# Kernel tuning notes

Hardware: AMD Instinct MI355X
Metric: run time of the kernel (lower is better)

Reference implementation:

```python
import jax, jax.numpy as jnp
import numpy as np
from jax import lax

D_MODEL = 512
CLASS_NUM = 8000
MAX_LEN = 80
VOCAB = 8002  # len(char2idx): chars + sos/eos
SOS_IDX = 0


def setup_inputs() -> dict:
    key = jax.random.key(0)
    ks = jax.random.split(key, 16)
    T, B, D, V, C = 128, 128, D_MODEL, VOCAB, CLASS_NUM
    s = 1.0 / np.sqrt(D)
    inp = {
        "inputs": jax.random.normal(ks[0], (T, B, D), jnp.float32),
        # additive attention params (query_size=key_size=hidden_size=D)
        "Wq": jax.random.normal(ks[1], (D, D), jnp.float32) * s,
        "bq": jnp.zeros((D,), jnp.float32),
        "Wk": jax.random.normal(ks[2], (D, D), jnp.float32) * s,
        "bk": jnp.zeros((D,), jnp.float32),
        "v": jax.random.normal(ks[3], (D,), jnp.float32) * s,
        # GRUCell: input_size = 2*D, hidden_size = D (PyTorch layout)
        "W_ih": jax.random.normal(ks[4], (3 * D, 2 * D), jnp.float32) * s,
        "b_ih": jnp.zeros((3 * D,), jnp.float32),
        "W_hh": jax.random.normal(ks[5], (3 * D, D), jnp.float32) * s,
        "b_hh": jnp.zeros((3 * D,), jnp.float32),
        # embedding table and classifier
        "emb": jax.random.normal(ks[6], (V, D), jnp.float32),
        "Wc": jax.random.normal(ks[7], (C, D), jnp.float32) * s,
        "bc": jnp.zeros((C,), jnp.float32),
    }
    return inp


def _gru_cell(x, h, W_ih, b_ih, W_hh, b_hh):
    # PyTorch GRUCell math
    gi = x @ W_ih.T + b_ih  # [B, 3D]
    gh = h @ W_hh.T + b_hh  # [B, 3D]
    i_r, i_z, i_n = jnp.split(gi, 3, axis=1)
    h_r, h_z, h_n = jnp.split(gh, 3, axis=1)
    r = jax.nn.sigmoid(i_r + h_r)
    z = jax.nn.sigmoid(i_z + h_z)
    n = jnp.tanh(i_n + r * h_n)
    return (1.0 - z) * n + z * h


def reference(inputs, Wq, bq, Wk, bk, v, W_ih, b_ih, W_hh, b_hh, emb, Wc, bc):
    T, B, D = inputs.shape
    # Attention is called as attention(inputs, keys) with keys = inputs each
    # step -> weights are loop-invariant; compute the context once.
    e = jnp.tanh(inputs @ Wq.T + bq + inputs @ Wk.T + bk) @ v  # [T, B]
    att = jax.nn.softmax(e, axis=0)[..., None]  # [T, B, 1]
    c = jnp.sum(att * inputs, axis=0)  # [B, D]

    h0 = inputs[0]  # initial GRU hidden = first encoder frame
    out0 = emb[jnp.full((B,), SOS_IDX, dtype=jnp.int32)]  # sos embedding

    def step(carry, _):
        h, out = carry
        x = jnp.concatenate([out, c], axis=1)  # [B, 2D]
        h = _gru_cell(x, h, W_ih, b_ih, W_hh, b_hh)
        pred = h @ Wc.T + bc  # [B, class_num]
        top1 = jnp.argmax(pred, axis=1)  # greedy decode (eval mode)
        return (h, emb[top1]), pred

    _, preds = lax.scan(step, (h0, out0), None, length=MAX_LEN)
    return preds  # [max_len, B, class_num]
```

## Files before the change

kernel.cpp:

```cpp
#include <hip/hip_runtime.h>
#include <cstdint>
#include <cstddef>

#define D_MOD 512
#define TH3   1536
#define CLS   8000
#define MAXLEN 80
#define B_SZ  128
#define T_LEN 128
#define NK0   16
#define EGI_ROWS 8000

typedef __attribute__((ext_vector_type(8))) __bf16 bf16x8;
typedef __attribute__((ext_vector_type(8))) unsigned short u16x8;
typedef __attribute__((ext_vector_type(4))) float f32x4;

__device__ __forceinline__ unsigned short f2bf(float x) {
    unsigned u = __float_as_uint(x);
    unsigned r = ((u >> 16) & 1u) + 0x7fffu;
    return (unsigned short)((u + r) >> 16);
}
__device__ __forceinline__ float bf2f(unsigned short h) {
    return __uint_as_float(((unsigned)h) << 16);
}
__device__ __forceinline__ f32x4 mfma16(u16x8 a, u16x8 b, f32x4 c) {
    return __builtin_amdgcn_mfma_f32_16x16x32_bf16(
        __builtin_bit_cast(bf16x8, a), __builtin_bit_cast(bf16x8, b), c, 0, 0, 0);
}
__device__ __forceinline__ void conv8(const float* __restrict__ p, u16x8& hi, u16x8& lo) {
    float4 f0 = *(const float4*)p;
    float4 f1 = *(const float4*)(p + 4);
    float fs[8] = {f0.x, f0.y, f0.z, f0.w, f1.x, f1.y, f1.z, f1.w};
    #pragma unroll
    for (int j = 0; j < 8; ++j) {
        unsigned short h = f2bf(fs[j]);
        hi[j] = h;
        lo[j] = f2bf(fs[j] - bf2f(h));
    }
}
__device__ __forceinline__ unsigned long long packkey(float v, int n) {
    unsigned u = __float_as_uint(v);
    u = (u & 0x80000000u) ? ~u : (u | 0x80000000u);
    return ((unsigned long long)u << 32) | (unsigned)(~(unsigned)n);
}
__device__ __forceinline__ unsigned long long shfl_xor_u64(unsigned long long x, int mask) {
    unsigned lo = (unsigned)x, hi = (unsigned)(x >> 32);
    lo = __shfl_xor(lo, mask, 16);
    hi = __shfl_xor(hi, mask, 16);
    return ((unsigned long long)hi << 32) | lo;
}
__device__ __forceinline__ size_t pk_off(int n, int k) {
    int tile = n >> 4, lr = n & 15, k0i = k >> 5, lk = (k >> 3) & 3, e = k & 7;
    return ((size_t)(tile * NK0 + k0i) * 64 + (lk * 16 + lr)) * 8 + e;
}

__global__ __launch_bounds__(256) void cvt2p_kernel(
    const float* __restrict__ s1, const float* __restrict__ s2, int ld,
    long total4, unsigned short* __restrict__ hi, unsigned short* __restrict__ lo)
{
    long i4 = (long)blockIdx.x * 256 + threadIdx.x;
    if (i4 >= total4) return;
    long r = i4 >> 7;
    int c = (int)(i4 & 127) * 4;
    float4 a = *(const float4*)(s1 + r * (long)ld + c);
    if (s2) {
        float4 b = *(const float4*)(s2 + r * (long)ld + c);
        a.x += b.x; a.y += b.y; a.z += b.z; a.w += b.w;
    }
    float xs[4] = {a.x, a.y, a.z, a.w};
    unsigned short hs[4], ls[4];
    #pragma unroll
    for (int j = 0; j < 4; ++j) {
        hs[j] = f2bf(xs[j]);
        ls[j] = f2bf(xs[j] - bf2f(hs[j]));
    }
    size_t o = pk_off((int)r, c);
    *(ushort4*)(hi + o) = make_ushort4(hs[0], hs[1], hs[2], hs[3]);
    *(ushort4*)(lo + o) = make_ushort4(ls[0], ls[1], ls[2], ls[3]);
}

template<bool GATHER_CONV, bool CONVB, bool ADD2D, bool ARGMAX, int NS, int KS>
__device__ __forceinline__ void gemm_ks2(
    float* __restrict__ red,
    const unsigned short* __restrict__ Ahi, const unsigned short* __restrict__ Alo,
    const float* __restrict__ Afp, const unsigned long long* __restrict__ gslot,
    const unsigned short* __restrict__ Bhi, const unsigned short* __restrict__ Blo,
    const float* __restrict__ Bfp,
    const float* __restrict__ bias, const float* __restrict__ D2,
    float* __restrict__ C, int ldc,
    unsigned long long* __restrict__ aslot, int bx, int by)
{
    static_assert(NS * KS == 8, "8 waves per block");
    const int tid = threadIdx.x;
    const int w = tid >> 6, lane = tid & 63;
    const int lr = lane & 15, lk = lane >> 4;
    const int ns = w % NS, ks = w / NS;
    const int m0 = by * 16;
    const int n0 = (bx * NS + ns) * 32;
    const int tA = by;
    const int tB0 = n0 >> 4, tB1 = tB0 + 1;

    const float* paf = nullptr;
    if constexpr (GATHER_CONV) {
        int g = gslot ? (int)(~(unsigned)gslot[m0 + lr]) : (m0 + lr);
        paf = Afp + (size_t)g * D_MOD + lk * 8;
    }
    const float *pb0f = nullptr, *pb1f = nullptr;
    if constexpr (CONVB) {
        pb0f = Bfp + (size_t)(n0 + lr) * D_MOD + lk * 8;
        pb1f = Bfp + (size_t)(n0 + 16 + lr) * D_MOD + lk * 8;
    }

    f32x4 acc0 = (f32x4){0.f, 0.f, 0.f, 0.f};
    f32x4 acc1 = (f32x4){0.f, 0.f, 0.f, 0.f};

    const int kBeg = ks * (NK0 / KS), kEnd = kBeg + (NK0 / KS);
    for (int k0i = kBeg; k0i < kEnd; ++k0i) {
        u16x8 ah, al, b0h, b0l, b1h, b1l;
        if constexpr (GATHER_CONV) {
            conv8(paf + k0i * 32, ah, al);
        } else {
            size_t oA = ((size_t)(tA * NK0 + k0i) * 64 + lane) * 8;
            ah = *(const u16x8*)(Ahi + oA); al = *(const u16x8*)(Alo + oA);
        }
        if constexpr (CONVB) {
            conv8(pb0f + k0i * 32, b0h, b0l);
            conv8(pb1f + k0i * 32, b1h, b1l);
        } else {
            size_t oB0 = ((size_t)(tB0 * NK0 + k0i) * 64 + lane) * 8;
            size_t oB1 = ((size_t)(tB1 * NK0 + k0i) * 64 + lane) * 8;
            b0h = *(const u16x8*)(Bhi + oB0); b0l = *(const u16x8*)(Blo + oB0);
            b1h = *(const u16x8*)(Bhi + oB1); b1l = *(const u16x8*)(Blo + oB1);
        }
        acc0 = mfma16(ah, b0h, acc0);
        acc0 = mfma16(ah, b0l, acc0);
        acc0 = mfma16(al, b0h, acc0);
        acc1 = mfma16(ah, b1h, acc1);
        acc1 = mfma16(ah, b1l, acc1);
        acc1 = mfma16(al, b1h, acc1);
    }

    float af[8];
    #pragma unroll
    for (int i = 0; i < 4; ++i) { af[i] = acc0[i]; af[4 + i] = acc1[i]; }

    if (ks > 0) {
        const int slot = (ks - 1) * NS + ns;
        #pragma unroll
        for (int i = 0; i < 8; ++i) red[slot * 576 + lane * 9 + i] = af[i];
    }
    __syncthreads();
    if (ks == 0) {
        #pragma unroll
        for (int j = 1; j < KS; ++j) {
            const int slot = (j - 1) * NS + ns;
            #pragma unroll
            for (int i = 0; i < 8; ++i) af[i] += red[slot * 576 + lane * 9 + i];
        }
        #pragma unroll
        for (int r = 0; r < 4; ++r) {
            const int row = m0 + lk * 4 + r;
            unsigned long long kmax = 0ull;
            #pragma unroll
            for (int ni = 0; ni < 2; ++ni) {
                const int col = n0 + ni * 16 + lr;
                float val = af[ni * 4 + r];
                if (bias) val += bias[col];
                if constexpr (ADD2D) val += D2[(size_t)row * ldc + col];
                C[(size_t)row * ldc + col] = val;
                if constexpr (ARGMAX) {
                    unsigned long long k = packkey(val, col);
                    if (k > kmax) kmax = k;
                }
            }
            if constexpr (ARGMAX) {
                #pragma unroll
                for (int off = 1; off < 16; off <<= 1) {
                    unsigned long long o = shfl_xor_u64(kmax, off);
                    if (o > kmax) kmax = o;
                }
                if (lr == 0) atomicMax(&aslot[row], kmax);
            }
        }
    }
}

template<int G>
__device__ __forceinline__ bool xcd_map(int p, int& bx, int& by) {
    int x = p & 7, s = p >> 3;
    by = s & 7;
    bx = x * G + (s >> 3);
    return true;
}

__global__ __launch_bounds__(512) void egi_kernel(
    const float* __restrict__ emb,
    const unsigned short* __restrict__ WihaHi, const unsigned short* __restrict__ WihaLo,
    float* __restrict__ Egi)
{
    __shared__ float red[7 * 576];
    int p = blockIdx.x;
    int x = p & 7, s = p >> 3;
    int by = s % 500, bx = x * 6 + s / 500;
    gemm_ks2<true, false, false, false, 1, 8>(red, nullptr, nullptr, emb, nullptr,
        WihaHi, WihaLo, nullptr, nullptr, nullptr, Egi, TH3, nullptr, bx, by);
}

__global__ __launch_bounds__(512) void gh_kernel(
    const unsigned short* __restrict__ hHi, const unsigned short* __restrict__ hLo,
    const unsigned short* __restrict__ WhhHi, const unsigned short* __restrict__ WhhLo,
    const float* __restrict__ b_hh, float* __restrict__ gh)
{
    __shared__ float red[7 * 576];
    int bx, by;
    xcd_map<6>(blockIdx.x, bx, by);
    gemm_ks2<false, false, false, false, 1, 8>(red, hHi, hLo, nullptr, nullptr,
        WhhHi, WhhLo, nullptr, b_hh, nullptr, gh, TH3, nullptr, bx, by);
}

template<bool CONVB>
__global__ __launch_bounds__(512) void cls_gh_kernel(
    const unsigned short* __restrict__ hHi, const unsigned short* __restrict__ hLo,
    const unsigned short* __restrict__ WcHi, const unsigned short* __restrict__ WcLo,
    const float* __restrict__ Wc, const float* __restrict__ bc,
    float* __restrict__ C, unsigned long long* __restrict__ aslot,
    const unsigned short* __restrict__ WhhHi, const unsigned short* __restrict__ WhhLo,
    const float* __restrict__ b_hh, float* __restrict__ gh)
{
    __shared__ float red[7 * 576];
    const int p = blockIdx.x;
    if (p < 1024) {
        int bx, by;
        xcd_map<16>(p, bx, by);
        if (bx >= 125) return;
        gemm_ks2<false, CONVB, false, true, 2, 4>(red, hHi, hLo, nullptr, nullptr,
            WcHi, WcLo, Wc, bc, nullptr, C, CLS, aslot, bx, by);
    } else {
        int bx, by;
        xcd_map<6>(p - 1024, bx, by);
        gemm_ks2<false, false, false, false, 1, 8>(red, hHi, hLo, nullptr, nullptr,
            WhhHi, WhhLo, nullptr, b_hh, nullptr, gh, TH3, nullptr, bx, by);
    }
}

__global__ __launch_bounds__(512) void step_dual_kernel(
    const unsigned short* __restrict__ hHi, const unsigned short* __restrict__ hLo,
    const unsigned short* __restrict__ WhhHi, const unsigned short* __restrict__ WhhLo,
    const float* __restrict__ b_hh,
    const float* __restrict__ emb, const unsigned long long* __restrict__ sPrev,
    const unsigned short* __restrict__ WihaHi, const unsigned short* __restrict__ WihaLo,
    const float* __restrict__ gc,
    float* __restrict__ gh, float* __restrict__ gi)
{
    __shared__ float red[7 * 576];
    int p = blockIdx.x;
    const int z = (p >= 384);
    p -= z * 384;
    int bx, by;
    xcd_map<6>(p, bx, by);
    if (z == 0)
        gemm_ks2<false, false, false, false, 1, 8>(red, hHi, hLo, nullptr, nullptr,
            WhhHi, WhhLo, nullptr, b_hh, nullptr, gh, TH3, nullptr, bx, by);
    else
        gemm_ks2<true, false, true, false, 1, 8>(red, nullptr, nullptr, emb, sPrev,
            WihaHi, WihaLo, nullptr, nullptr, gc, gi, TH3, nullptr, bx, by);
}

__global__ __launch_bounds__(512) void gemm128_kernel(
    const unsigned short* __restrict__ Ahi, const unsigned short* __restrict__ Alo,
    const unsigned short* __restrict__ Bhi, const unsigned short* __restrict__ Blo,
    const float* __restrict__ bias, float* __restrict__ C)
{
    __shared__ float red[7 * 576];
    int bx, by;
    xcd_map<6>(blockIdx.x, bx, by);
    gemm_ks2<false, false, false, false, 1, 8>(red, Ahi, Alo, nullptr, nullptr,
        Bhi, Blo, nullptr, bias, nullptr, C, TH3, nullptr, bx, by);
}

template<bool CONVB>
__global__ __launch_bounds__(512) void cls_kernel(
    const unsigned short* __restrict__ hHi, const unsigned short* __restrict__ hLo,
    const unsigned short* __restrict__ WcHi, const unsigned short* __restrict__ WcLo,
    const float* __restrict__ Wc, const float* __restrict__ bc,
    float* __restrict__ C, unsigned long long* __restrict__ aslot)
{
    __shared__ float red[3 * 2 * 576];
    int bx, by;
    xcd_map<16>(blockIdx.x, bx, by);
    if (bx >= 125) return;
    gemm_ks2<false, CONVB, false, true, 2, 4>(red, hHi, hLo, nullptr, nullptr,
        WcHi, WcLo, Wc, bc, nullptr, C, CLS, aslot, bx, by);
}

__global__ __launch_bounds__(256) void attn_e_mfma(
    const float* __restrict__ inp,
    const unsigned short* __restrict__ WqkHi, const unsigned short* __restrict__ WqkLo,
    const float* __restrict__ bq, const float* __restrict__ bk,
    const float* __restrict__ v, float* __restrict__ e)
{
    __shared__ __align__(16) unsigned short Ah[32][40];
    __shared__ __align__(16) unsigned short Al[32][40];
    __shared__ float red[4][32];
    const int tid = threadIdx.x, w = tid >> 6, lane = tid & 63;
    const int lr = lane & 15, lk = lane >> 4;
    const int m0 = blockIdx.x * 32;
    const int srow = tid >> 3, scol = (tid & 7) * 4;

    f32x4 acc[2][8];
    #pragma unroll
    for (int i = 0; i < 2; ++i)
        #pragma unroll
        for (int j = 0; j < 8; ++j) acc[i][j] = (f32x4){0.f, 0.f, 0.f, 0.f};

    for (int k0i = 0; k0i < NK0; ++k0i) {
        float4 x = *(const float4*)(inp + (size_t)(m0 + srow) * D_MOD + k0i * 32 + scol);
        float xs[4] = {x.x, x.y, x.z, x.w};
        #pragma unroll
        for (int j = 0; j < 4; ++j) {
            unsigned short h = f2bf(xs[j]);
            Ah[srow][scol + j] = h;
            Al[srow][scol + j] = f2bf(xs[j] - bf2f(h));
        }
        __syncthreads();
        u16x8 a[2][2];
        #pragma unroll
        for (int mi = 0; mi < 2; ++mi) {
            a[mi][0] = *(const u16x8*)&Ah[mi * 16 + lr][lk * 8];
            a[mi][1] = *(const u16x8*)&Al[mi * 16 + lr][lk * 8];
        }
        #pragma unroll
        for (int nf = 0; nf < 8; ++nf) {
            const int tile = w * 8 + nf;
            size_t ob = ((size_t)(tile * NK0 + k0i) * 64 + lane) * 8;
            u16x8 bh = *(const u16x8*)(WqkHi + ob);
            u16x8 bl = *(const u16x8*)(WqkLo + ob);
            #pragma unroll
            for (int mi = 0; mi < 2; ++mi) {
                acc[mi][nf] = mfma16(a[mi][0], bh, acc[mi][nf]);
                acc[mi][nf] = mfma16(a[mi][0], bl, acc[mi][nf]);
                acc[mi][nf] = mfma16(a[mi][1], bh, acc[mi][nf]);
            }
        }
        __syncthreads();
    }

    float ep[2][4];
    #pragma unroll
    for (int mi = 0; mi < 2; ++mi)
        #pragma unroll
        for (int r = 0; r < 4; ++r) ep[mi][r] = 0.f;
    #pragma unroll
    for (int nf = 0; nf < 8; ++nf) {
        const int col = w * 128 + nf * 16 + lr;
        const float bb = bq[col] + bk[col];
        const float vv = v[col];
        #pragma unroll
        for (int mi = 0; mi < 2; ++mi)
            #pragma unroll
            for (int r = 0; r < 4; ++r)
                ep[mi][r] += vv * tanhf(acc[mi][nf][r] + bb);
    }
    #pragma unroll
    for (int mi = 0; mi < 2; ++mi)
        #pragma unroll
        for (int r = 0; r < 4; ++r) {
            float s = ep[mi][r];
            #pragma unroll
            for (int off = 1; off < 16; off <<= 1) s += __shfl_xor(s, off, 16);
            if (lr == 0) red[w][mi * 16 + lk * 4 + r] = s;
        }
    __syncthreads();
    if (tid < 32) e[m0 + tid] = red[0][tid] + red[1][tid] + red[2][tid] + red[3][tid];
}

__global__ __launch_bounds__(256) void softmax_ctx_kernel(
    const float* __restrict__ inp, const float* __restrict__ e,
    unsigned short* __restrict__ cHi, unsigned short* __restrict__ cLo,
    float* __restrict__ h1, unsigned short* __restrict__ h1Hi, unsigned short* __restrict__ h1Lo,
    unsigned long long* __restrict__ slots)
{
    __shared__ float att[T_LEN];
    __shared__ float red;
    const int b = blockIdx.x, tid = threadIdx.x;
    float val = -1e30f;
    if (tid < T_LEN) { val = e[(size_t)tid * B_SZ + b]; att[tid] = val; }
    __syncthreads();
    if (tid < 64) {
        float m = fmaxf(att[tid], att[tid + 64]);
        #pragma unroll
        for (int off = 32; off; off >>= 1) m = fmaxf(m, __shfl_xor(m, off));
        if (tid == 0) red = m;
    }
    __syncthreads();
    const float mx = red;
    __syncthreads();
    if (tid < T_LEN) att[tid] = expf(val - mx);
    __syncthreads();
    if (tid < 64) {
        float s = att[tid] + att[tid + 64];
        #pragma unroll
        for (int off = 32; off; off >>= 1) s += __shfl_xor(s, off);
        if (tid == 0) red = s;
    }
    __syncthreads();
    const float inv = 1.f / red;

    const int d0 = tid * 2;
    float ax = 0.f, ay = 0.f;
    for (int t = 0; t < T_LEN; ++t) {
        float a = att[t];
        float2 x = *(const float2*)(inp + ((size_t)t * B_SZ + b) * D_MOD + d0);
        ax += a * x.x; ay += a * x.y;
        if (t == 0) {
            *(float2*)(h1 + (size_t)b * D_MOD + d0) = x;
            unsigned short hx = f2bf(x.x), hy = f2bf(x.y);
            h1Hi[pk_off(b, d0)]     = hx;
            h1Hi[pk_off(b, d0 + 1)] = hy;
            h1Lo[pk_off(b, d0)]     = f2bf(x.x - bf2f(hx));
            h1Lo[pk_off(b, d0 + 1)] = f2bf(x.y - bf2f(hy));
        }
    }
    ax *= inv; ay *= inv;
    unsigned short cx = f2bf(ax), cy = f2bf(ay);
    cHi[pk_off(b, d0)]     = cx;
    cHi[pk_off(b, d0 + 1)] = cy;
    cLo[pk_off(b, d0)]     = f2bf(ax - bf2f(cx));
    cLo[pk_off(b, d0 + 1)] = f2bf(ay - bf2f(cy));
    if (tid == 0) {
        slots[b] = 0ull;
        slots[B_SZ + b] = 0x00000000FFFFFFFFull;
    }
}

__global__ __launch_bounds__(512) void gru_combine(
    const float* __restrict__ gh, const float* __restrict__ gi,
    const float* __restrict__ hPrev, float* __restrict__ hCur,
    unsigned short* __restrict__ hHiC, unsigned short* __restrict__ hLoC,
    unsigned long long* __restrict__ slotCur)
{
    const int b = blockIdx.x, k = threadIdx.x;
    const float* gib = gi + (size_t)b * TH3;
    const float* ghb = gh + (size_t)b * TH3;
    float r = 1.f / (1.f + expf(-(gib[k] + ghb[k])));
    float z = 1.f / (1.f + expf(-(gib[k + 512] + ghb[k + 512])));
    float n = tanhf(gib[k + 1024] + r * ghb[k + 1024]);
    float h = hPrev[(size_t)b * D_MOD + k];
    float hv = (1.f - z) * n + z * h;
    hCur[(size_t)b * D_MOD + k] = hv;
    unsigned short hh = f2bf(hv);
    size_t o = pk_off(b, k);
    hHiC[o] = hh;
    hLoC[o] = f2bf(hv - bf2f(hh));
    if (k == 0) slotCur[b] = 0ull;
}

__global__ __launch_bounds__(512) void gru_combine_egi(
    const float* __restrict__ gh, const float* __restrict__ Egi,
    const float* __restrict__ gc, const unsigned long long* __restrict__ sPrev,
    const float* __restrict__ hPrev, float* __restrict__ hCur,
    unsigned short* __restrict__ hHiC, unsigned short* __restrict__ hLoC,
    unsigned long long* __restrict__ slotCur)
{
    const int b = blockIdx.x, k = threadIdx.x;
    const int sel = (int)(~(unsigned)sPrev[b]);
    const float* gib = Egi + (size_t)sel * TH3;
    const float* gcb = gc + (size_t)b * TH3;
    const float* ghb = gh + (size_t)b * TH3;
    float gi0 = gib[k] + gcb[k];
    float gi1 = gib[k + 512] + gcb[k + 512];
    float gi2 = gib[k + 1024] + gcb[k + 1024];
    float r = 1.f / (1.f + expf(-(gi0 + ghb[k])));
    float z = 1.f / (1.f + expf(-(gi1 + ghb[k + 512])));
    float n = tanhf(gi2 + r * ghb[k + 1024]);
    float h = hPrev[(size_t)b * D_MOD + k];
    float hv = (1.f - z) * n + z * h;
    hCur[(size_t)b * D_MOD + k] = hv;
    unsigned short hh = f2bf(hv);
    size_t o = pk_off(b, k);
    hHiC[o] = hh;
    hLoC[o] = f2bf(hv - bf2f(hh));
    if (k == 0) slotCur[b] = 0ull;
}

extern "C" void kernel_launch(void* const* d_in, const int* in_sizes, int n_in,
                              void* d_out, int out_size, void* d_ws, size_t ws_size,
                              hipStream_t stream)
{
    const float* inp  = (const float*)d_in[0];
    const float* Wq   = (const float*)d_in[1];
    const float* bq   = (const float*)d_in[2];
    const float* Wk   = (const float*)d_in[3];
    const float* bk   = (const float*)d_in[4];
    const float* v    = (const float*)d_in[5];
    const float* W_ih = (const float*)d_in[6];
    const float* b_ih = (const float*)d_in[7];
    const float* W_hh = (const float*)d_in[8];
    const float* b_hh = (const float*)d_in[9];
    const float* emb  = (const float*)d_in[10];
    const float* Wc   = (const float*)d_in[11];
    const float* bc   = (const float*)d_in[12];
    float* out = (float*)d_out;

    char* base = (char*)d_ws;
    size_t off = 0;
    auto alloc = [&](size_t bytes) -> char* {
        char* q = base + off;
        off += (bytes + 255) & ~(size_t)255;
        return q;
    };
    typedef unsigned short us;
    us* WqkHi  = (us*)alloc(512 * 512 * 2);
    us* WqkLo  = (us*)alloc(512 * 512 * 2);
    us* WhhHi  = (us*)alloc((size_t)TH3 * 512 * 2);
    us* WhhLo  = (us*)alloc((size_t)TH3 * 512 * 2);
    us* WihaHi = (us*)alloc((size_t)TH3 * 512 * 2);
    us* WihaLo = (us*)alloc((size_t)TH3 * 512 * 2);
    us* WihbHi = (us*)alloc((size_t)TH3 * 512 * 2);
    us* WihbLo = (us*)alloc((size_t)TH3 * 512 * 2);
    float* e   = (float*)alloc(T_LEN * B_SZ * 4);
    us* cHi    = (us*)alloc(B_SZ * 512 * 2);
    us* cLo    = (us*)alloc(B_SZ * 512 * 2);
    float* gc  = (float*)alloc((size_t)B_SZ * TH3 * 4);
    float* gh  = (float*)alloc((size_t)B_SZ * TH3 * 4);
    float* gi  = (float*)alloc((size_t)B_SZ * TH3 * 4);
    float* hF[2]; us* hHi[2]; us* hLo[2];
    hF[0] = (float*)alloc(B_SZ * 512 * 4);
    hF[1] = (float*)alloc(B_SZ * 512 * 4);
    hHi[0] = (us*)alloc(B_SZ * 512 * 2);
    hHi[1] = (us*)alloc(B_SZ * 512 * 2);
    hLo[0] = (us*)alloc(B_SZ * 512 * 2);
    hLo[1] = (us*)alloc(B_SZ * 512 * 2);
    unsigned long long* slots = (unsigned long long*)alloc(2 * B_SZ * 8);
    us* WcHi = (us*)alloc((size_t)CLS * 512 * 2);
    us* WcLo = (us*)alloc((size_t)CLS * 512 * 2);
    const bool PREB = (off <= ws_size);
    float* Egi = (float*)alloc((size_t)EGI_ROWS * TH3 * 4);
    const bool EGIB = (off <= ws_size);

    cvt2p_kernel<<<(512 * 128) / 256, 256, 0, stream>>>(Wq, Wk, 512, 512L * 128, WqkHi, WqkLo);
    cvt2p_kernel<<<(TH3 * 128) / 256, 256, 0, stream>>>(W_hh, nullptr, 512, (long)TH3 * 128, WhhHi, WhhLo);
    cvt2p_kernel<<<(TH3 * 128) / 256, 256, 0, stream>>>(W_ih, nullptr, 1024, (long)TH3 * 128, WihaHi, WihaLo);
    cvt2p_kernel<<<(TH3 * 128) / 256, 256, 0, stream>>>(W_ih + 512, nullptr, 1024, (long)TH3 * 128, WihbHi, WihbLo);
    if (PREB)
        cvt2p_kernel<<<(CLS * 128) / 256, 256, 0, stream>>>(Wc, nullptr, 512, (long)CLS * 128, WcHi, WcLo);
    if (EGIB)
        egi_kernel<<<8 * 6 * 500, 512, 0, stream>>>(emb, WihaHi, WihaLo, Egi);

    attn_e_mfma<<<(T_LEN * B_SZ) / 32, 256, 0, stream>>>(inp, WqkHi, WqkLo, bq, bk, v, e);
    softmax_ctx_kernel<<<B_SZ, 256, 0, stream>>>(inp, e, cHi, cLo, hF[1], hHi[1], hLo[1], slots);
    gemm128_kernel<<<384, 512, 0, stream>>>(cHi, cLo, WihbHi, WihbLo, b_ih, gc);

    if (EGIB) {
        gh_kernel<<<384, 512, 0, stream>>>(hHi[1], hLo[1], WhhHi, WhhLo, b_hh, gh);
        for (int t = 0; t < MAXLEN; ++t) {
            const int pi = (t + 1) & 1, ci = t & 1;
            unsigned long long* sPrev = slots + pi * B_SZ;
            unsigned long long* sCur  = slots + ci * B_SZ;

            gru_combine_egi<<<B_SZ, 512, 0, stream>>>(
                gh, Egi, gc, sPrev, hF[pi], hF[ci], hHi[ci], hLo[ci], sCur);
            if (PREB)
                cls_gh_kernel<false><<<1408, 512, 0, stream>>>(
                    hHi[ci], hLo[ci], WcHi, WcLo, nullptr, bc,
                    out + (size_t)t * B_SZ * CLS, sCur,
                    WhhHi, WhhLo, b_hh, gh);
            else
                cls_gh_kernel<true><<<1408, 512, 0, stream>>>(
                    hHi[ci], hLo[ci], nullptr, nullptr, Wc, bc,
                    out + (size_t)t * B_SZ * CLS, sCur,
                    WhhHi, WhhLo, b_hh, gh);
        }
    } else {
        for (int t = 0; t < MAXLEN; ++t) {
            const int pi = (t + 1) & 1, ci = t & 1;
            unsigned long long* sPrev = slots + pi * B_SZ;
            unsigned long long* sCur  = slots + ci * B_SZ;

            step_dual_kernel<<<768, 512, 0, stream>>>(
                hHi[pi], hLo[pi], WhhHi, WhhLo, b_hh,
                emb, sPrev, WihaHi, WihaLo, gc, gh, gi);
            gru_combine<<<B_SZ, 512, 0, stream>>>(
                gh, gi, hF[pi], hF[ci], hHi[ci], hLo[ci], sCur);
            if (PREB)
                cls_kernel<false><<<1024, 512, 0, stream>>>(
                    hHi[ci], hLo[ci], WcHi, WcLo, nullptr, bc,
                    out + (size_t)t * B_SZ * CLS, sCur);
            else
                cls_kernel<true><<<1024, 512, 0, stream>>>(
                    hHi[ci], hLo[ci], nullptr, nullptr, Wc, bc,
                    out + (size_t)t * B_SZ * CLS, sCur);
        }
    }
}
```

Baseline: 2.615 ms.

## Tile multiple M sub-tiles per wave in classifier GEMM and use nontemporal stores

Templates the shared split-K MFMA GEMM on an M-tile count so each wave computes several 16-row tiles and reuses each loaded B fragment across them. A new fused classifier plus hidden-projection kernel with 608 blocks replaces the 1408-block launch when both precomputed buffers fit, which cuts repeated reads of the large Wc weights. Output logits can be written with nontemporal stores so they do not evict weights from cache. In exchange each wave holds more accumulators and uses more reduction shared memory, which can lower occupancy.

```diff
diff --git a/kernel.cpp b/kernel.cpp
--- a/kernel.cpp
+++ b/kernel.cpp
@@ -79,7 +79,8 @@
     *(ushort4*)(lo + o) = make_ushort4(ls[0], ls[1], ls[2], ls[3]);
 }
 
-template<bool GATHER_CONV, bool CONVB, bool ADD2D, bool ARGMAX, int NS, int KS>
+template<bool GATHER_CONV, bool CONVB, bool ADD2D, bool ARGMAX, bool NT,
+         int NS, int KS, int MT>
 __device__ __forceinline__ void gemm_ks2(
     float* __restrict__ red,
     const unsigned short* __restrict__ Ahi, const unsigned short* __restrict__ Alo,
@@ -91,13 +92,14 @@
     unsigned long long* __restrict__ aslot, int bx, int by)
 {
     static_assert(NS * KS == 8, "8 waves per block");
+    static_assert(!GATHER_CONV || MT == 1, "gather path is MT=1 only");
     const int tid = threadIdx.x;
     const int w = tid >> 6, lane = tid & 63;
     const int lr = lane & 15, lk = lane >> 4;
     const int ns = w % NS, ks = w / NS;
-    const int m0 = by * 16;
+    const int m0 = by * (16 * MT);
     const int n0 = (bx * NS + ns) * 32;
-    const int tA = by;
+    const int tA0 = by * MT;
     const int tB0 = n0 >> 4, tB1 = tB0 + 1;
 
     const float* paf = nullptr;
@@ -111,17 +113,25 @@
         pb1f = Bfp + (size_t)(n0 + 16 + lr) * D_MOD + lk * 8;
     }
 
-    f32x4 acc0 = (f32x4){0.f, 0.f, 0.f, 0.f};
-    f32x4 acc1 = (f32x4){0.f, 0.f, 0.f, 0.f};
+    f32x4 acc[MT][2];
+    #pragma unroll
+    for (int mi = 0; mi < MT; ++mi) {
+        acc[mi][0] = (f32x4){0.f, 0.f, 0.f, 0.f};
+        acc[mi][1] = (f32x4){0.f, 0.f, 0.f, 0.f};
+    }
 
     const int kBeg = ks * (NK0 / KS), kEnd = kBeg + (NK0 / KS);
     for (int k0i = kBeg; k0i < kEnd; ++k0i) {
-        u16x8 ah, al, b0h, b0l, b1h, b1l;
+        u16x8 ah[MT], al[MT], b0h, b0l, b1h, b1l;
         if constexpr (GATHER_CONV) {
-            conv8(paf + k0i * 32, ah, al);
+            conv8(paf + k0i * 32, ah[0], al[0]);
         } else {
-            size_t oA = ((size_t)(tA * NK0 + k0i) * 64 + lane) * 8;
-            ah = *(const u16x8*)(Ahi + oA); al = *(const u16x8*)(Alo + oA);
+            #pragma unroll
+            for (int mi = 0; mi < MT; ++mi) {
+                size_t oA = ((size_t)((tA0 + mi) * NK0 + k0i) * 64 + lane) * 8;
+                ah[mi] = *(const u16x8*)(Ahi + oA);
+                al[mi] = *(const u16x8*)(Alo + oA);
+            }
         }
         if constexpr (CONVB) {
             conv8(pb0f + k0i * 32, b0h, b0l);
@@ -132,22 +142,30 @@
             b0h = *(const u16x8*)(Bhi + oB0); b0l = *(const u16x8*)(Blo + oB0);
             b1h = *(const u16x8*)(Bhi + oB1); b1l = *(const u16x8*)(Blo + oB1);
         }
-        acc0 = mfma16(ah, b0h, acc0);
-        acc0 = mfma16(ah, b0l, acc0);
-        acc0 = mfma16(al, b0h, acc0);
-        acc1 = mfma16(ah, b1h, acc1);
-        acc1 = mfma16(ah, b1l, acc1);
-        acc1 = mfma16(al, b1h, acc1);
-    }
-
-    float af[8];
-    #pragma unroll
-    for (int i = 0; i < 4; ++i) { af[i] = acc0[i]; af[4 + i] = acc1[i]; }
+        #pragma unroll
+        for (int mi = 0; mi < MT; ++mi) {
+            acc[mi][0] = mfma16(ah[mi], b0h, acc[mi][0]);
+            acc[mi][0] = mfma16(ah[mi], b0l, acc[mi][0]);
+            acc[mi][0] = mfma16(al[mi], b0h, acc[mi][0]);
+            acc[mi][1] = mfma16(ah[mi], b1h, acc[mi][1]);
+            acc[mi][1] = mfma16(ah[mi], b1l, acc[mi][1]);
+            acc[mi][1] = mfma16(al[mi], b1h, acc[mi][1]);
+        }
+    }
+
+    float af[MT][8];
+    #pragma unroll
+    for (int mi = 0; mi < MT; ++mi)
+        #pragma unroll
+        for (int i = 0; i < 4; ++i) { af[mi][i] = acc[mi][0][i]; af[mi][4 + i] = acc[mi][1][i]; }
 
     if (ks > 0) {
         const int slot = (ks - 1) * NS + ns;
         #pragma unroll
-        for (int i = 0; i < 8; ++i) red[slot * 576 + lane * 9 + i] = af[i];
+        for (int mi = 0; mi < MT; ++mi)
+            #pragma unroll
+            for (int i = 0; i < 8; ++i)
+                red[(slot * MT + mi) * 576 + lane * 9 + i] = af[mi][i];
     }
     __syncthreads();
     if (ks == 0) {
@@ -155,31 +173,38 @@
         for (int j = 1; j < KS; ++j) {
             const int slot = (j - 1) * NS + ns;
             #pragma unroll
-            for (int i = 0; i < 8; ++i) af[i] += red[slot * 576 + lane * 9 + i];
-        }
-        #pragma unroll
-        for (int r = 0; r < 4; ++r) {
-            const int row = m0 + lk * 4 + r;
-            unsigned long long kmax = 0ull;
+            for (int mi = 0; mi < MT; ++mi)
+                #pragma unroll
+                for (int i = 0; i < 8; ++i)
+                    af[mi][i] += red[(slot * MT + mi) * 576 + lane * 9 + i];
+        }
+        #pragma unroll
+        for (int mi = 0; mi < MT; ++mi) {
             #pragma unroll
-            for (int ni = 0; ni < 2; ++ni) {
-                const int col = n0 + ni * 16 + lr;
-                float val = af[ni * 4 + r];
-                if (bias) val += bias[col];
-                if constexpr (ADD2D) val += D2[(size_t)row * ldc + col];
-                C[(size_t)row * ldc + col] = val;
+            for (int r = 0; r < 4; ++r) {
+                const int row = m0 + mi * 16 + lk * 4 + r;
+                unsigned long long kmax = 0ull;
+                #pragma unroll
+                for (int ni = 0; ni < 2; ++ni) {
+                    const int col = n0 + ni * 16 + lr;
+                    float val = af[mi][ni * 4 + r];
+                    if (bias) val += bias[col];
+                    if constexpr (ADD2D) val += D2[(size_t)row * ldc + col];
+                    if constexpr (NT) __builtin_nontemporal_store(val, &C[(size_t)row * ldc + col]);
+                    else C[(size_t)row * ldc + col] = val;
+                    if constexpr (ARGMAX) {
+                        unsigned long long k = packkey(val, col);
+                        if (k > kmax) kmax = k;
+                    }
+                }
                 if constexpr (ARGMAX) {
-                    unsigned long long k = packkey(val, col);
-                    if (k > kmax) kmax = k;
+                    #pragma unroll
+                    for (int off = 1; off < 16; off <<= 1) {
+                        unsigned long long o = shfl_xor_u64(kmax, off);
+                        if (o > kmax) kmax = o;
+                    }
+                    if (lr == 0) atomicMax(&aslot[row], kmax);
                 }
-            }
-            if constexpr (ARGMAX) {
-                #pragma unroll
-                for (int off = 1; off < 16; off <<= 1) {
-                    unsigned long long o = shfl_xor_u64(kmax, off);
-                    if (o > kmax) kmax = o;
-                }
-                if (lr == 0) atomicMax(&aslot[row], kmax);
             }
         }
     }
@@ -193,276 +218,14 @@
     return true;
 }
 
-__global__ __launch_bounds__(512) void egi_kernel(
-    const float* __restrict__ emb,
-    const unsigned short* __restrict__ WihaHi, const unsigned short* __restrict__ WihaLo,
-    float* __restrict__ Egi)
-{
-    __shared__ float red[7 * 576];
-    int p = blockIdx.x;
-    int x = p & 7, s = p >> 3;
-    int by = s % 500, bx = x * 6 + s / 500;
-    gemm_ks2<true, false, false, false, 1, 8>(red, nullptr, nullptr, emb, nullptr,
-        WihaHi, WihaLo, nullptr, nullptr, nullptr, Egi, TH3, nullptr, bx, by);
-}
-
-__global__ __launch_bounds__(512) void gh_kernel(
-    const unsigned short* __restrict__ hHi, const unsigned short* __restrict__ hLo,
-    const unsigned short* __restrict__ WhhHi, const unsigned short* __restrict__ WhhLo,
-    const float* __restrict__ b_hh, float* __restrict__ gh)
-{
-    __shared__ float red[7 * 576];
-    int bx, by;
-    xcd_map<6>(blockIdx.x, bx, by);
-    gemm_ks2<false, false, false, false, 1, 8>(red, hHi, hLo, nullptr, nullptr,
-        WhhHi, WhhLo, nullptr, b_hh, nullptr, gh, TH3, nullptr, bx, by);
-}
-
-template<bool CONVB>
-__global__ __launch_bounds__(512) void cls_gh_kernel(
-    const unsigned short* __restrict__ hHi, const unsigned short* __restrict__ hLo,
-    const unsigned short* __restrict__ WcHi, const unsigned short* __restrict__ WcLo,
-    const float* __restrict__ Wc, const float* __restrict__ bc,
-    float* __restrict__ C, unsigned long long* __restrict__ aslot,
-    const unsigned short* __restrict__ WhhHi, const unsigned short* __restrict__ WhhLo,
-    const float* __restrict__ b_hh, float* __restrict__ gh)
-{
-    __shared__ float red[7 * 576];
-    const int p = blockIdx.x;
-    if (p < 1024) {
-        int bx, by;
-        xcd_map<16>(p, bx, by);
-        if (bx >= 125) return;
-        gemm_ks2<false, CONVB, false, true, 2, 4>(red, hHi, hLo, nullptr, nullptr,
-            WcHi, WcLo, Wc, bc, nullptr, C, CLS, aslot, bx, by);
-    } else {
-        int bx, by;
-        xcd_map<6>(p - 1024, bx, by);
-        gemm_ks2<false, false, false, false, 1, 8>(red, hHi, hLo, nullptr, nullptr,
-            WhhHi, WhhLo, nullptr, b_hh, nullptr, gh, TH3, nullptr, bx, by);
-    }
-}
-
-__global__ __launch_bounds__(512) void step_dual_kernel(
-    const unsigned short* __restrict__ hHi, const unsigned short* __restrict__ hLo,
-    const unsigned short* __restrict__ WhhHi, const unsigned short* __restrict__ WhhLo,
-    const float* __restrict__ b_hh,
-    const float* __restrict__ emb, const unsigned long long* __restrict__ sPrev,
-    const unsigned short* __restrict__ WihaHi, const unsigned short* __restrict__ WihaLo,
-    const float* __restrict__ gc,
-    float* __restrict__ gh, float* __restrict__ gi)
-{
-    __shared__ float red[7 * 576];
-    int p = blockIdx.x;
-    const int z = (p >= 384);
-    p -= z * 384;
-    int bx, by;
-    xcd_map<6>(p, bx, by);
-    if (z == 0)
-        gemm_ks2<false, false, false, false, 1, 8>(red, hHi, hLo, nullptr, nullptr,
-            WhhHi, WhhLo, nullptr, b_hh, nullptr, gh, TH3, nullptr, bx, by);
-    else
-        gemm_ks2<true, false, true, false, 1, 8>(red, nullptr, nullptr, emb, sPrev,
-            WihaHi, WihaLo, nullptr, nullptr, gc, gi, TH3, nullptr, bx, by);
-}
-
-__global__ __launch_bounds__(512) void gemm128_kernel(
-    const unsigned short* __restrict__ Ahi, const unsigned short* __restrict__ Alo,
-    const unsigned short* __restrict__ Bhi, const unsigned short* __restrict__ Blo,
-    const float* __restrict__ bias, float* __restrict__ C)
-{
-    __shared__ float red[7 * 576];
-    int bx, by;
-    xcd_map<6>(blockIdx.x, bx, by);
-    gemm_ks2<false, false, false, false, 1, 8>(red, Ahi, Alo, nullptr, nullptr,
-        Bhi, Blo, nullptr, bias, nullptr, C, TH3, nullptr, bx, by);
-}
-
-template<bool CONVB>
-__global__ __launch_bounds__(512) void cls_kernel(
-    const unsigned short* __restrict__ hHi, const unsigned short* __restrict__ hLo,
-    const unsigned short* __restrict__ WcHi, const unsigned short* __restrict__ WcLo,
-    const float* __restrict__ Wc, const float* __restrict__ bc,
-    float* __restrict__ C, unsigned long long* __restrict__ aslot)
-{
-    __shared__ float red[3 * 2 * 576];
-    int bx, by;
-    xcd_map<16>(blockIdx.x, bx, by);
-    if (bx >= 125) return;
-    gemm_ks2<false, CONVB, false, true, 2, 4>(red, hHi, hLo, nullptr, nullptr,
-        WcHi, WcLo, Wc, bc, nullptr, C, CLS, aslot, bx, by);
-}
-
-__global__ __launch_bounds__(256) void attn_e_mfma(
-    const float* __restrict__ inp,
-    const unsigned short* __restrict__ WqkHi, const unsigned short* __restrict__ WqkLo,
-    const float* __restrict__ bq, const float* __restrict__ bk,
-    const float* __restrict__ v, float* __restrict__ e)
-{
-    __shared__ __align__(16) unsigned short Ah[32][40];
-    __shared__ __align__(16) unsigned short Al[32][40];
-    __shared__ float red[4][32];
-    const int tid = threadIdx.x, w = tid >> 6, lane = tid & 63;
-    const int lr = lane & 15, lk = lane >> 4;
-    const int m0 = blockIdx.x * 32;
-    const int srow = tid >> 3, scol = (tid & 7) * 4;
-
-    f32x4 acc[2][8];
-    #pragma unroll
-    for (int i = 0; i < 2; ++i)
-        #pragma unroll
-        for (int j = 0; j < 8; ++j) acc[i][j] = (f32x4){0.f, 0.f, 0.f, 0.f};
-
-    for (int k0i = 0; k0i < NK0; ++k0i) {
-        float4 x = *(const float4*)(inp + (size_t)(m0 + srow) * D_MOD + k0i * 32 + scol);
-        float xs[4] = {x.x, x.y, x.z, x.w};
-        #pragma unroll
-        for (int j = 0; j < 4; ++j) {
-            unsigned short h = f2bf(xs[j]);
-            Ah[srow][scol + j] = h;
-            Al[srow][scol + j] = f2bf(xs[j] - bf2f(h));
-        }
-        __syncthreads();
-        u16x8 a[2][2];
-        #pragma unroll
-        for (int mi = 0; mi < 2; ++mi) {
-            a[mi][0] = *(const u16x8*)&Ah[mi * 16 + lr][lk * 8];
-            a[mi][1] = *(const u16x8*)&Al[mi * 16 + lr][lk * 8];
-        }
-        #pragma unroll
-        for (int nf = 0; nf < 8; ++nf) {
-            const int tile = w * 8 + nf;
-            size_t ob = ((size_t)(tile * NK0 + k0i) * 64 + lane) * 8;
-            u16x8 bh = *(const u16x8*)(WqkHi + ob);
-            u16x8 bl = *(const u16x8*)(WqkLo + ob);
-            #pragma unroll
-            for (int mi = 0; mi < 2; ++mi) {
-                acc[mi][nf] = mfma16(a[mi][0], bh, acc[mi][nf]);
-                acc[mi][nf] = mfma16(a[mi][0], bl, acc[mi][nf]);
-                acc[mi][nf] = mfma16(a[mi][1], bh, acc[mi][nf]);
-            }
-        }
-        __syncthreads();
-    }
-
-    float ep[2][4];
-    #pragma unroll
-    for (int mi = 0; mi < 2; ++mi)
-        #pragma unroll
-        for (int r = 0; r < 4; ++r) ep[mi][r] = 0.f;
-    #pragma unroll
-    for (int nf = 0; nf < 8; ++nf) {
-        const int col = w * 128 + nf * 16 + lr;
-        const float bb = bq[col] + bk[col];
-        const float vv = v[col];
-        #pragma unroll
-        for (int mi = 0; mi < 2; ++mi)
-            #pragma unroll
-            for (int r = 0; r < 4; ++r)
-                ep[mi][r] += vv * tanhf(acc[mi][nf][r] + bb);
-    }
-    #pragma unroll
-    for (int mi = 0; mi < 2; ++mi)
-        #pragma unroll
-        for (int r = 0; r < 4; ++r) {
-            float s = ep[mi][r];
-            #pragma unroll
-            for (int off = 1; off < 16; off <<= 1) s += __shfl_xor(s, off, 16);
-            if (lr == 0) red[w][mi * 16 + lk * 4 + r] = s;
-        }
-    __syncthreads();
-    if (tid < 32) e[m0 + tid] = red[0][tid] + red[1][tid] + red[2][tid] + red[3][tid];
-}
-
-__global__ __launch_bounds__(256) void softmax_ctx_kernel(
-    const float* __restrict__ inp, const float* __restrict__ e,
-    unsigned short* __restrict__ cHi, unsigned short* __restrict__ cLo,
-    float* __restrict__ h1, unsigned short* __restrict__ h1Hi, unsigned short* __restrict__ h1Lo,
-    unsigned long long* __restrict__ slots)
-{
-    __shared__ float att[T_LEN];
-    __shared__ float red;
-    const int b = blockIdx.x, tid = threadIdx.x;
-    float val = -1e30f;
-    if (tid < T_LEN) { val = e[(size_t)tid * B_SZ + b]; att[tid] = val; }
-    __syncthreads();
-    if (tid < 64) {
-        float m = fmaxf(att[tid], att[tid + 64]);
-        #pragma unroll
-        for (int off = 32; off; off >>= 1) m = fmaxf(m, __shfl_xor(m, off));
-        if (tid == 0) red = m;
-    }
-    __syncthreads();
-    const float mx = red;
-    __syncthreads();
-    if (tid < T_LEN) att[tid] = expf(val - mx);
-    __syncthreads();
-    if (tid < 64) {
-        float s = att[tid] + att[tid + 64];
-        #pragma unroll
-        for (int off = 32; off; off >>= 1) s += __shfl_xor(s, off);
-        if (tid == 0) red = s;
-    }
-    __syncthreads();
-    const float inv = 1.f / red;
-
-    const int d0 = tid * 2;
-    float ax = 0.f, ay = 0.f;
-    for (int t = 0; t < T_LEN; ++t) {
-        float a = att[t];
-        float2 x = *(const float2*)(inp + ((size_t)t * B_SZ + b) * D_MOD + d0);
-        ax += a * x.x; ay += a * x.y;
-        if (t == 0) {
-            *(float2*)(h1 + (size_t)b * D_MOD + d0) = x;
-            unsigned short hx = f2bf(x.x), hy = f2bf(x.y);
-            h1Hi[pk_off(b, d0)]     = hx;
-            h1Hi[pk_off(b, d0 + 1)] = hy;
-            h1Lo[pk_off(b, d0)]     = f2bf(x.x - bf2f(hx));
-            h1Lo[pk_off(b, d0 + 1)] = f2bf(x.y - bf2f(hy));
-        }
-    }
-    ax *= inv; ay *= inv;
-    unsigned short cx = f2bf(ax), cy = f2bf(ay);
-    cHi[pk_off(b, d0)]     = cx;
-    cHi[pk_off(b, d0 + 1)] = cy;
-    cLo[pk_off(b, d0)]     = f2bf(ax - bf2f(cx));
-    cLo[pk_off(b, d0 + 1)] = f2bf(ay - bf2f(cy));
-    if (tid == 0) {
-        slots[b] = 0ull;
-        slots[B_SZ + b] = 0x00000000FFFFFFFFull;
-    }
-}
-
-__global__ __launch_bounds__(512) void gru_combine(
-    const float* __restrict__ gh, const float* __restrict__ gi,
-    const float* __restrict__ hPrev, float* __restrict__ hCur,
-    unsigned short* __restrict__ hHiC, unsigned short* __restrict__ hLoC,
-    unsigned long long* __restrict__ slotCur)
-{
-    const int b = blockIdx.x, k = threadIdx.x;
-    const float* gib = gi + (size_t)b * TH3;
-    const float* ghb = gh + (size_t)b * TH3;
-    float r = 1.f / (1.f + expf(-(gib[k] + ghb[k])));
-    float z = 1.f / (1.f + expf(-(gib[k + 512] + ghb[k + 512])));
-    float n = tanhf(gib[k + 1024] + r * ghb[k + 1024]);
-    float h = hPrev[(size_t)b * D_MOD + k];
-    float hv = (1.f - z) * n + z * h;
-    hCur[(size_t)b * D_MOD + k] = hv;
-    unsigned short hh = f2bf(hv);
-    size_t o = pk_off(b, k);
-    hHiC[o] = hh;
-    hLoC[o] = f2bf(hv - bf2f(hh));
-    if (k == 0) slotCur[b] = 0ull;
-}
-
-__global__ __launch_bounds__(512) void gru_combine_egi(
-    const float* __restrict__ gh, const float* __restrict__ Egi,
+__device__ __forceinline__ void gru_job_egi(
+    int b, const float* __restrict__ gh, const float* __restrict__ Egi,
     const float* __restrict__ gc, const unsigned long long* __restrict__ sPrev,
     const float* __restrict__ hPrev, float* __restrict__ hCur,
     unsigned short* __restrict__ hHiC, unsigned short* __restrict__ hLoC,
     unsigned long long* __restrict__ slotCur)
 {
-    const int b = blockIdx.x, k = threadIdx.x;
+    const int k = threadIdx.x;
     const int sel = (int)(~(unsigned)sPrev[b]);
     const float* gib = Egi + (size_t)sel * TH3;
     const float* gcb = gc + (size_t)b * TH3;
@@ -481,6 +244,303 @@
     hHiC[o] = hh;
     hLoC[o] = f2bf(hv - bf2f(hh));
     if (k == 0) slotCur[b] = 0ull;
+}
+
+__global__ __launch_bounds__(512) void egi_kernel(
+    const float* __restrict__ emb,
+    const unsigned short* __restrict__ WihaHi, const unsigned short* __restrict__ WihaLo,
+    float* __restrict__ Egi)
+{
+    __shared__ float red[7 * 576];
+    int p = blockIdx.x;
+    int x = p & 7, s = p >> 3;
+    int by = s % 500, bx = x * 6 + s / 500;
+    gemm_ks2<true, false, false, false, false, 1, 8, 1>(red, nullptr, nullptr,
+        emb, nullptr, WihaHi, WihaLo, nullptr, nullptr, nullptr, Egi, TH3, nullptr, bx, by);
+}
+
+__global__ __launch_bounds__(512) void gh_kernel(
+    const unsigned short* __restrict__ hHi, const unsigned short* __restrict__ hLo,
+    const unsigned short* __restrict__ WhhHi, const unsigned short* __restrict__ WhhLo,
+    const float* __restrict__ b_hh, float* __restrict__ gh)
+{
+    __shared__ float red[7 * 576];
+    int bx, by;
+    xcd_map<6>(blockIdx.x, bx, by);
+    gemm_ks2<false, false, false, false, false, 1, 8, 1>(red, hHi, hLo, nullptr, nullptr,
+        WhhHi, WhhLo, nullptr, b_hh, nullptr, gh, TH3, nullptr, bx, by);
+}
+
+__global__ __launch_bounds__(512, 6) void clsgh2_kernel(
+    const unsigned short* __restrict__ hHi, const unsigned short* __restrict__ hLo,
+    const unsigned short* __restrict__ WcHi, const unsigned short* __restrict__ WcLo,
+    const float* __restrict__ bc,
+    float* __restrict__ C, unsigned long long* __restrict__ aslot,
+    const unsigned short* __restrict__ WhhHi, const unsigned short* __restrict__ WhhLo,
+    const float* __restrict__ b_hh, float* __restrict__ gh)
+{
+    __shared__ float red[3 * 2 * 2 * 576];
+    const int p = blockIdx.x;
+    if (p < 512) {
+        int x = p & 7, s = p >> 3;
+        int by = s & 3, bx = x * 16 + (s >> 2);
+        if (bx >= 125) return;
+        gemm_ks2<false, false, false, true, true, 2, 4, 2>(red, hHi, hLo, nullptr, nullptr,
+            WcHi, WcLo, nullptr, bc, nullptr, C, CLS, aslot, bx, by);
+    } else {
+        int q = p - 512;
+        int x = q & 7, s = q >> 3;
+        int by = s & 3, bx = x * 3 + (s >> 2);
+        gemm_ks2<false, false, false, false, false, 2, 4, 2>(red, hHi, hLo, nullptr, nullptr,
+            WhhHi, WhhLo, nullptr, b_hh, nullptr, gh, TH3, nullptr, bx, by);
+    }
+}
+
+template<bool CONVB>
+__global__ __launch_bounds__(512) void cls_gh_kernel(
+    const unsigned short* __restrict__ hHi, const unsigned short* __restrict__ hLo,
+    const unsigned short* __restrict__ WcHi, const unsigned short* __restrict__ WcLo,
+    const float* __restrict__ Wc, const float* __restrict__ bc,
+    float* __restrict__ C, unsigned long long* __restrict__ aslot,
+    const unsigned short* __restrict__ WhhHi, const unsigned short* __restrict__ WhhLo,
+    const float* __restrict__ b_hh, float* __restrict__ gh)
+{
+    __shared__ float red[7 * 576];
+    const int p = blockIdx.x;
+    if (p < 1024) {
+        int bx, by;
+        xcd_map<16>(p, bx, by);
+        if (bx >= 125) return;
+        gemm_ks2<false, CONVB, false, true, false, 2, 4, 1>(red, hHi, hLo, nullptr, nullptr,
+            WcHi, WcLo, Wc, bc, nullptr, C, CLS, aslot, bx, by);
+    } else {
+        int bx, by;
+        xcd_map<6>(p - 1024, bx, by);
+        gemm_ks2<false, false, false, false, false, 1, 8, 1>(red, hHi, hLo, nullptr, nullptr,
+            WhhHi, WhhLo, nullptr, b_hh, nullptr, gh, TH3, nullptr, bx, by);
+    }
+}
+
+__global__ __launch_bounds__(512) void step_dual_kernel(
+    const unsigned short* __restrict__ hHi, const unsigned short* __restrict__ hLo,
+    const unsigned short* __restrict__ WhhHi, const unsigned short* __restrict__ WhhLo,
+    const float* __restrict__ b_hh,
+    const float* __restrict__ emb, const unsigned long long* __restrict__ sPrev,
+    const unsigned short* __restrict__ WihaHi, const unsigned short* __restrict__ WihaLo,
+    const float* __restrict__ gc,
+    float* __restrict__ gh, float* __restrict__ gi)
+{
+    __shared__ float red[7 * 576];
+    int p = blockIdx.x;
+    const int z = (p >= 384);
+    p -= z * 384;
+    int bx, by;
+    xcd_map<6>(p, bx, by);
+    if (z == 0)
+        gemm_ks2<false, false, false, false, false, 1, 8, 1>(red, hHi, hLo, nullptr, nullptr,
+            WhhHi, WhhLo, nullptr, b_hh, nullptr, gh, TH3, nullptr, bx, by);
+    else
+        gemm_ks2<true, false, true, false, false, 1, 8, 1>(red, nullptr, nullptr, emb, sPrev,
+            WihaHi, WihaLo, nullptr, nullptr, gc, gi, TH3, nullptr, bx, by);
+}
+
+__global__ __launch_bounds__(512) void gemm128_kernel(
+    const unsigned short* __restrict__ Ahi, const unsigned short* __restrict__ Alo,
+    const unsigned short* __restrict__ Bhi, const unsigned short* __restrict__ Blo,
+    const float* __restrict__ bias, float* __restrict__ C)
+{
+    __shared__ float red[7 * 576];
+    int bx, by;
+    xcd_map<6>(blockIdx.x, bx, by);
+    gemm_ks2<false, false, false, false, false, 1, 8, 1>(red, Ahi, Alo, nullptr, nullptr,
+        Bhi, Blo, nullptr, bias, nullptr, C, TH3, nullptr, bx, by);
+}
+
+template<bool CONVB>
+__global__ __launch_bounds__(512) void cls_kernel(
+    const unsigned short* __restrict__ hHi, const unsigned short* __restrict__ hLo,
+    const unsigned short* __restrict__ WcHi, const unsigned short* __restrict__ WcLo,
+    const float* __restrict__ Wc, const float* __restrict__ bc,
+    float* __restrict__ C, unsigned long long* __restrict__ aslot)
+{
+    __shared__ float red[3 * 2 * 576];
+    int bx, by;
+    xcd_map<16>(blockIdx.x, bx, by);
+    if (bx >= 125) return;
+    gemm_ks2<false, CONVB, false, true, false, 2, 4, 1>(red, hHi, hLo, nullptr, nullptr,
+        WcHi, WcLo, Wc, bc, nullptr, C, CLS, aslot, bx, by);
+}
+
+__global__ __launch_bounds__(256) void attn_e_mfma(
+    const float* __restrict__ inp,
+    const unsigned short* __restrict__ WqkHi, const unsigned short* __restrict__ WqkLo,
+    const float* __restrict__ bq, const float* __restrict__ bk,
+    const float* __restrict__ v, float* __restrict__ e)
+{
+    __shared__ __align__(16) unsigned short Ah[32][40];
+    __shared__ __align__(16) unsigned short Al[32][40];
+    __shared__ float red[4][32];
+    const int tid = threadIdx.x, w = tid >> 6, lane = tid & 63;
+    const int lr = lane & 15, lk = lane >> 4;
+    const int m0 = blockIdx.x * 32;
+    const int srow = tid >> 3, scol = (tid & 7) * 4;
+
+    f32x4 acc[2][8];
+    #pragma unroll
+    for (int i = 0; i < 2; ++i)
+        #pragma unroll
+        for (int j = 0; j < 8; ++j) acc[i][j] = (f32x4){0.f, 0.f, 0.f, 0.f};
+
+    for (int k0i = 0; k0i < NK0; ++k0i) {
+        float4 x = *(const float4*)(inp + (size_t)(m0 + srow) * D_MOD + k0i * 32 + scol);
+        float xs[4] = {x.x, x.y, x.z, x.w};
+        #pragma unroll
+        for (int j = 0; j < 4; ++j) {
+            unsigned short h = f2bf(xs[j]);
+            Ah[srow][scol + j] = h;
+            Al[srow][scol + j] = f2bf(xs[j] - bf2f(h));
+        }
+        __syncthreads();
+        u16x8 a[2][2];
+        #pragma unroll
+        for (int mi = 0; mi < 2; ++mi) {
+            a[mi][0] = *(const u16x8*)&Ah[mi * 16 + lr][lk * 8];
+            a[mi][1] = *(const u16x8*)&Al[mi * 16 + lr][lk * 8];
+        }
+        #pragma unroll
+        for (int nf = 0; nf < 8; ++nf) {
+            const int tile = w * 8 + nf;
+            size_t ob = ((size_t)(tile * NK0 + k0i) * 64 + lane) * 8;
+            u16x8 bh = *(const u16x8*)(WqkHi + ob);
+            u16x8 bl = *(const u16x8*)(WqkLo + ob);
+            #pragma unroll
+            for (int mi = 0; mi < 2; ++mi) {
+                acc[mi][nf] = mfma16(a[mi][0], bh, acc[mi][nf]);
+                acc[mi][nf] = mfma16(a[mi][0], bl, acc[mi][nf]);
+                acc[mi][nf] = mfma16(a[mi][1], bh, acc[mi][nf]);
+            }
+        }
+        __syncthreads();
+    }
+
+    float ep[2][4];
+    #pragma unroll
+    for (int mi = 0; mi < 2; ++mi)
+        #pragma unroll
+        for (int r = 0; r < 4; ++r) ep[mi][r] = 0.f;
+    #pragma unroll
+    for (int nf = 0; nf < 8; ++nf) {
+        const int col = w * 128 + nf * 16 + lr;
+        const float bb = bq[col] + bk[col];
+        const float vv = v[col];
+        #pragma unroll
+        for (int mi = 0; mi < 2; ++mi)
+            #pragma unroll
+            for (int r = 0; r < 4; ++r)
+                ep[mi][r] += vv * tanhf(acc[mi][nf][r] + bb);
+    }
+    #pragma unroll
+    for (int mi = 0; mi < 2; ++mi)
+        #pragma unroll
+        for (int r = 0; r < 4; ++r) {
+            float s = ep[mi][r];
+            #pragma unroll
+            for (int off = 1; off < 16; off <<= 1) s += __shfl_xor(s, off, 16);
+            if (lr == 0) red[w][mi * 16 + lk * 4 + r] = s;
+        }
+    __syncthreads();
+    if (tid < 32) e[m0 + tid] = red[0][tid] + red[1][tid] + red[2][tid] + red[3][tid];
+}
+
+__global__ __launch_bounds__(256) void softmax_ctx_kernel(
+    const float* __restrict__ inp, const float* __restrict__ e,
+    unsigned short* __restrict__ cHi, unsigned short* __restrict__ cLo,
+    float* __restrict__ h1, unsigned short* __restrict__ h1Hi, unsigned short* __restrict__ h1Lo,
+    unsigned long long* __restrict__ slots)
+{
+    __shared__ float att[T_LEN];
+    __shared__ float red;
+    const int b = blockIdx.x, tid = threadIdx.x;
+    float val = -1e30f;
+    if (tid < T_LEN) { val = e[(size_t)tid * B_SZ + b]; att[tid] = val; }
+    __syncthreads();
+    if (tid < 64) {
+        float m = fmaxf(att[tid], att[tid + 64]);
+        #pragma unroll
+        for (int off = 32; off; off >>= 1) m = fmaxf(m, __shfl_xor(m, off));
+        if (tid == 0) red = m;
+    }
+    __syncthreads();
+    const float mx = red;
+    __syncthreads();
+    if (tid < T_LEN) att[tid] = expf(val - mx);
+    __syncthreads();
+    if (tid < 64) {
+        float s = att[tid] + att[tid + 64];
+        #pragma unroll
+        for (int off = 32; off; off >>= 1) s += __shfl_xor(s, off);
+        if (tid == 0) red = s;
+    }
+    __syncthreads();
+    const float inv = 1.f / red;
+
+    const int d0 = tid * 2;
+    float ax = 0.f, ay = 0.f;
+    for (int t = 0; t < T_LEN; ++t) {
+        float a = att[t];
+        float2 x = *(const float2*)(inp + ((size_t)t * B_SZ + b) * D_MOD + d0);
+        ax += a * x.x; ay += a * x.y;
+        if (t == 0) {
+            *(float2*)(h1 + (size_t)b * D_MOD + d0) = x;
+            unsigned short hx = f2bf(x.x), hy = f2bf(x.y);
+            h1Hi[pk_off(b, d0)]     = hx;
+            h1Hi[pk_off(b, d0 + 1)] = hy;
+            h1Lo[pk_off(b, d0)]     = f2bf(x.x - bf2f(hx));
+            h1Lo[pk_off(b, d0 + 1)] = f2bf(x.y - bf2f(hy));
+        }
+    }
+    ax *= inv; ay *= inv;
+    unsigned short cx = f2bf(ax), cy = f2bf(ay);
+    cHi[pk_off(b, d0)]     = cx;
+    cHi[pk_off(b, d0 + 1)] = cy;
+    cLo[pk_off(b, d0)]     = f2bf(ax - bf2f(cx));
+    cLo[pk_off(b, d0 + 1)] = f2bf(ay - bf2f(cy));
+    if (tid == 0) {
+        slots[b] = 0ull;
+        slots[B_SZ + b] = 0x00000000FFFFFFFFull;
+    }
+}
+
+__global__ __launch_bounds__(512) void gru_combine(
+    const float* __restrict__ gh, const float* __restrict__ gi,
+    const float* __restrict__ hPrev, float* __restrict__ hCur,
+    unsigned short* __restrict__ hHiC, unsigned short* __restrict__ hLoC,
+    unsigned long long* __restrict__ slotCur)
+{
+    const int b = blockIdx.x, k = threadIdx.x;
+    const float* gib = gi + (size_t)b * TH3;
+    const float* ghb = gh + (size_t)b * TH3;
+    float r = 1.f / (1.f + expf(-(gib[k] + ghb[k])));
+    float z = 1.f / (1.f + expf(-(gib[k + 512] + ghb[k + 512])));
+    float n = tanhf(gib[k + 1024] + r * ghb[k + 1024]);
+    float h = hPrev[(size_t)b * D_MOD + k];
+    float hv = (1.f - z) * n + z * h;
+    hCur[(size_t)b * D_MOD + k] = hv;
+    unsigned short hh = f2bf(hv);
+    size_t o = pk_off(b, k);
+    hHiC[o] = hh;
+    hLoC[o] = f2bf(hv - bf2f(hh));
+    if (k == 0) slotCur[b] = 0ull;
+}
+
+__global__ __launch_bounds__(512) void gru_combine_egi(
+    const float* __restrict__ gh, const float* __restrict__ Egi,
+    const float* __restrict__ gc, const unsigned long long* __restrict__ sPrev,
+    const float* __restrict__ hPrev, float* __restrict__ hCur,
+    unsigned short* __restrict__ hHiC, unsigned short* __restrict__ hLoC,
+    unsigned long long* __restrict__ slotCur)
+{
+    gru_job_egi(blockIdx.x, gh, Egi, gc, sPrev, hPrev, hCur, hHiC, hLoC, slotCur);
 }
 
 extern "C" void kernel_launch(void* const* d_in, const int* in_sizes, int n_in,
@@ -551,32 +611,36 @@
     softmax_ctx_kernel<<<B_SZ, 256, 0, stream>>>(inp, e, cHi, cLo, hF[1], hHi[1], hLo[1], slots);
     gemm128_kernel<<<384, 512, 0, stream>>>(cHi, cLo, WihbHi, WihbLo, b_ih, gc);
 
-    if (EGIB) {
+    if (EGIB && PREB) {
+        gh_kernel<<<384, 512, 0, stream>>>(hHi[1], hLo[1], WhhHi, WhhLo, b_hh, gh);
+        for (int t = 0; t < MAXLEN; ++t) {
+            const int pi = (t + 1) & 1, ci = t & 1;
+            gru_combine_egi<<<B_SZ, 512, 0, stream>>>(
+                gh, Egi, gc, slots + pi * B_SZ, hF[pi], hF[ci], hHi[ci], hLo[ci],
+                slots + ci * B_SZ);
+            clsgh2_kernel<<<608, 512, 0, stream>>>(
+                hHi[ci], hLo[ci], WcHi, WcLo, bc,
+                out + (size_t)t * B_SZ * CLS, slots + ci * B_SZ,
+                WhhHi, WhhLo, b_hh, gh);
+        }
+    } else if (EGIB) {
         gh_kernel<<<384, 512, 0, stream>>>(hHi[1], hLo[1], WhhHi, WhhLo, b_hh, gh);
         for (int t = 0; t < MAXLEN; ++t) {
             const int pi = (t + 1) & 1, ci = t & 1;
             unsigned long long* sPrev = slots + pi * B_SZ;
             unsigned long long* sCur  = slots + ci * B_SZ;
-
             gru_combine_egi<<<B_SZ, 512, 0, stream>>>(
                 gh, Egi, gc, sPrev, hF[pi], hF[ci], hHi[ci], hLo[ci], sCur);
-            if (PREB)
-                cls_gh_kernel<false><<<1408, 512, 0, stream>>>(
-                    hHi[ci], hLo[ci], WcHi, WcLo, nullptr, bc,
-                    out + (size_t)t * B_SZ * CLS, sCur,
-                    WhhHi, WhhLo, b_hh, gh);
-            else
-                cls_gh_kernel<true><<<1408, 512, 0, stream>>>(
-                    hHi[ci], hLo[ci], nullptr, nullptr, Wc, bc,
-                    out + (size_t)t * B_SZ * CLS, sCur,
-                    WhhHi, WhhLo, b_hh, gh);
+            cls_gh_kernel<true><<<1408, 512, 0, stream>>>(
+                hHi[ci], hLo[ci], nullptr, nullptr, Wc, bc,
+                out + (size_t)t * B_SZ * CLS, sCur,
+                WhhHi, WhhLo, b_hh, gh);
         }
     } else {
         for (int t = 0; t < MAXLEN; ++t) {
             const int pi = (t + 1) & 1, ci = t & 1;
             unsigned long long* sPrev = slots + pi * B_SZ;
             unsigned long long* sCur  = slots + ci * B_SZ;
-
             step_dual_kernel<<<768, 512, 0, stream>>>(
                 hHi[pi], hLo[pi], WhhHi, WhhLo, b_hh,
                 emb, sPrev, WihaHi, WihaLo, gc, gh, gi);
```

Result: slower. 2.755 ms (+5.4%).
